# Kernel tuning notes

Hardware: AMD Instinct MI355X
Metric: run time of the kernel (lower is better)

Reference implementation:

```python
import jax, jax.numpy as jnp
import numpy as np

THRESH = 0.5
LENS = 0.5
DECAY = 0.2
K = 3


def _edge_norm(src, dst, n):
    # symmetric GCN normalization D^{-1/2} A D^{-1/2} (in-degree on dst)
    deg = jnp.zeros((n,), jnp.float32).at[dst].add(1.0)
    dinv = jnp.where(deg > 0, deg ** -0.5, 0.0)
    return dinv[src] * dinv[dst]


def _tag_conv(x, src, dst, norm, w, b):
    feats = [x]
    h = x
    for _ in range(K):
        msgs = h[:, src, :] * norm[None, :, None]   # [B, E, C]
        h = jnp.zeros_like(h).at[:, dst, :].add(msgs)
        feats.append(h)
    return jnp.concatenate(feats, axis=-1) @ w + b


def _act(m):
    # ActFun forward: heaviside at thresh
    return (m > THRESH).astype(m.dtype)


def _forward(data, sp_ei, tm_ei, conv1_w, conv1_b, conv2_w, conv2_b,
             fc1_w, fc1_b, tfc1_w, tfc1_b, act):
    B = data.shape[0]
    T = data.shape[-1]
    NS = data.shape[1] // 2  # 39 taxels
    # cat((data[:, :39], data[:, 39:]), dim=-2) -> [B, 39, 4, T]
    merged = jnp.concatenate([data[:, :NS], data[:, NS:]], axis=2)
    src_s, dst_s = sp_ei[0], sp_ei[1]
    norm_s = _edge_norm(src_s, dst_s, NS)
    src_t, dst_t = tm_ei[0], tm_ei[1]
    norm_t = _edge_norm(src_t, dst_t, T)
    COUT = conv1_w.shape[1]
    NC = fc1_w.shape[1]

    def spatial_step(carry, x_t):
        c_mem, c_spk, h_mem, h_spk, h_sum = carry
        c_mem = c_mem * DECAY * (1.0 - c_spk) + _tag_conv(x_t, src_s, dst_s, norm_s, conv1_w, conv1_b)
        c_spk = act(c_mem)
        h_mem = h_mem * DECAY * (1.0 - h_spk) + c_spk.reshape(B, -1) @ fc1_w + fc1_b
        h_spk = act(h_mem)
        return (c_mem, c_spk, h_mem, h_spk, h_sum + h_spk), None

    init_s = (jnp.zeros((B, NS, COUT)), jnp.zeros((B, NS, COUT)),
              jnp.zeros((B, NC)), jnp.zeros((B, NC)), jnp.zeros((B, NC)))
    xs_s = jnp.moveaxis(merged, 3, 0)  # [T, B, 39, 4]
    (_, _, _, _, h_sum), _ = jax.lax.scan(spatial_step, init_s, xs_s)
    out_spatial = h_sum / T

    def temporal_step(carry, x_s):
        t_mem, t_spk, th_mem, th_spk, th_sum = carry
        t_mem = t_mem * DECAY * (1.0 - t_spk) + _tag_conv(x_s, src_t, dst_t, norm_t, conv2_w, conv2_b)
        t_spk = act(t_mem)
        th_mem = th_mem * DECAY * (1.0 - th_spk) + t_spk.reshape(B, -1) @ tfc1_w + tfc1_b
        th_spk = act(th_mem)
        return (t_mem, t_spk, th_mem, th_spk, th_sum + th_spk), None

    init_t = (jnp.zeros((B, T, COUT)), jnp.zeros((B, T, COUT)),
              jnp.zeros((B, NC)), jnp.zeros((B, NC)), jnp.zeros((B, NC)))
    xs_t = jnp.moveaxis(merged, 1, 0).transpose(0, 1, 3, 2)  # [39, B, 325, 4]
    (_, _, _, _, th_sum), _ = jax.lax.scan(temporal_step, init_t, xs_t)
    out_temporal = th_sum / NS

    return (out_spatial + out_temporal) / 2.0


def setup_inputs():
    key = jax.random.key(0)
    ks = jax.random.split(key, 8)
    B, T, NS, CIN, COUT, NC = 256, 325, 39, 4, 64, 20
    data = jax.random.normal(ks[0], (B, 2 * NS, 2, T), jnp.float32)
    spatial_edge_index = jax.random.randint(ks[1], (2, NS * 3), 0, NS)
    t = jnp.arange(T - 1)
    temporal_edge_index = jnp.concatenate(
        [jnp.stack([t, t + 1]), jnp.stack([t + 1, t])], axis=1)  # [2, 648] chain
    conv1_w = jax.random.normal(ks[2], ((K + 1) * CIN, COUT), jnp.float32) * 0.1
    conv1_b = jnp.zeros((COUT,), jnp.float32)
    conv2_w = jax.random.normal(ks[3], ((K + 1) * CIN, COUT), jnp.float32) * 0.1
    conv2_b = jnp.zeros((COUT,), jnp.float32)
    fc1_w = jax.random.normal(ks[4], (NS * COUT, NC), jnp.float32) * 0.02
    fc1_b = jnp.zeros((NC,), jnp.float32)
    tfc1_w = jax.random.normal(ks[5], (T * COUT, NC), jnp.float32) * 0.02
    tfc1_b = jnp.zeros((NC,), jnp.float32)
    return dict(data=data, spatial_edge_index=spatial_edge_index,
                temporal_edge_index=temporal_edge_index,
                conv1_w=conv1_w, conv1_b=conv1_b, conv2_w=conv2_w, conv2_b=conv2_b,
                fc1_w=fc1_w, fc1_b=fc1_b, tfc1_w=tfc1_w, tfc1_b=tfc1_b)


def reference(data, spatial_edge_index, temporal_edge_index, conv1_w, conv1_b,
              conv2_w, conv2_b, fc1_w, fc1_b, tfc1_w, tfc1_b):
    return _forward(data, spatial_edge_index, temporal_edge_index,
                    conv1_w, conv1_b, conv2_w, conv2_b,
                    fc1_w, fc1_b, tfc1_w, tfc1_b, _act)
```

## Files before the change

### kernel.cpp

```cpp
#include <hip/hip_runtime.h>

typedef unsigned int u32;
typedef unsigned long long u64;
typedef short bf16x8 __attribute__((ext_vector_type(8)));
typedef float f32x4 __attribute__((ext_vector_type(4)));

#define Bc 256
#define Tc 325
#define NSc 39
#define COc 64
#define NCc 20
#define ESc 117
#define ETc 648

#define WS_ROFF_S 0
#define WS_EDGE_S 64
#define WS_DINV_S 304
#define WS_ROFF_T 352
#define WS_EDGE_T 680
#define WS_DINV_T 1976
#define WS_W1T    2304
#define WS_W2T    52224

__global__ void prep_graph(const int* __restrict__ eiS, const int* __restrict__ eiT,
                           int* __restrict__ wsI, float* __restrict__ wsF) {
  const int which = blockIdx.x;
  const int* ei = which ? eiT : eiS;
  const int nE = which ? ETc : ESc;
  const int nN = which ? Tc : NSc;
  int* roff = wsI + (which ? WS_ROFF_T : WS_ROFF_S);
  int2* edge = (int2*)(wsI + (which ? WS_EDGE_T : WS_EDGE_S));
  float* dinv = wsF + (which ? WS_DINV_T : WS_DINV_S);
  const int* src = ei;
  const int* dst = ei + nE;
  for (int n = threadIdx.x; n < nN; n += blockDim.x) {
    int deg = 0, before = 0;
    for (int e = 0; e < nE; ++e) { deg += (dst[e] == n); before += (dst[e] < n); }
    roff[n] = before;
    if (n == nN - 1) roff[nN] = before + deg;
    dinv[n] = (deg > 0) ? (1.0f / sqrtf((float)deg)) : 0.0f;
  }
  __syncthreads();
  for (int n = threadIdx.x; n < nN; n += blockDim.x) {
    int cur = roff[n];
    float dn = dinv[n];
    for (int e = 0; e < nE; ++e) {
      if (dst[e] == n) {
        edge[cur] = make_int2(src[e], __float_as_int(dinv[src[e]] * dn));
        ++cur;
      }
    }
  }
}

__global__ void prep_w(const float* __restrict__ w1, float* __restrict__ w1T,
                       const float* __restrict__ w2, float* __restrict__ w2T) {
  int i = blockIdx.x * 256 + threadIdx.x;
  if (i < NCc * Tc * COc) {
    int j = i / (Tc * COc);
    int p = i - j * (Tc * COc);
    w2T[i] = w2[p * NCc + j];
  }
  if (i < NCc * NSc * COc) {
    int j = i / (NSc * COc);
    int p = i - j * (NSc * COc);
    w1T[i] = w1[p * NCc + j];
  }
}

__global__ __launch_bounds__(512) __attribute__((amdgpu_waves_per_eu(2, 2)))
void lif_fused(const float* __restrict__ data,
               const int* __restrict__ roffSg, const int2* __restrict__ edgeSg,
               const int* __restrict__ roffTg, const int2* __restrict__ edgeTg,
               const float* __restrict__ c1w, const float* __restrict__ c1b,
               const float* __restrict__ c2w, const float* __restrict__ c2b,
               const float* __restrict__ w1T, const float* __restrict__ f1b,
               const float* __restrict__ tf1w, const float* __restrict__ tf1b,
               float* __restrict__ out)
{
  __shared__ u64 spk[NSc * Tc];
  __shared__ __align__(16) float fAB[13000];
  __shared__ float partials[520];
  __shared__ float outS_l[NCc];
  __shared__ int roffS[NSc + 1];
  __shared__ int2 edgeS[ESc];
  __shared__ int roffT[Tc + 1];
  __shared__ int2 edgeT[ETc];

  const int tid = threadIdx.x;
  const int lane = tid & 63;
  const int wv = tid >> 6;
  const int b = blockIdx.x;
  const int lhalf = lane >> 5;
  const int lbit = lane & 31;
  const float* dbase = data + (size_t)b * (2 * NSc * 2 * Tc);

  for (int i = tid; i < NSc + 1; i += 512) roffS[i] = roffSg[i];
  for (int i = tid; i < ESc; i += 512) edgeS[i] = edgeSg[i];
  for (int i = tid; i < Tc + 1; i += 512) roffT[i] = roffTg[i];
  for (int i = tid; i < ETc; i += 512) edgeT[i] = edgeTg[i];

  const int jg = wv >> 1, ih = wv & 1;
  const int ja = wv, jb = wv + 8, jc = wv + 16;
  const int jag = ja / 5, jaj = ja % 5;
  const int jbg = jb / 5, jbj = jb % 5;
  const int jcg = jc / 5, jcj = jc % 5;

  {
    const float bcv = c1b[lane];
    float cm[5] = {0, 0, 0, 0, 0};
    const int iBase = ih * 20, iN = ih ? 19 : 20;
    const float* wq0 = w1T + (jg * 5 + 0) * (NSc * COc) + iBase * COc + lane;
    const float* wq1 = w1T + (jg * 5 + 1) * (NSc * COc) + iBase * COc + lane;
    const float* wq2 = w1T + (jg * 5 + 2) * (NSc * COc) + iBase * COc + lane;
    const float* wq3 = w1T + (jg * 5 + 3) * (NSc * COc) + iBase * COc + lane;
    const float* wq4 = w1T + (jg * 5 + 4) * (NSc * COc) + iBase * COc + lane;
    const float ba = f1b[ja], bb = f1b[jb];
    const float bc2 = (wv < 4) ? f1b[jc] : 0.0f;
    float hma = 0, hsa = 0, hmb = 0, hsb = 0, hmc = 0, hsc = 0;
    __syncthreads();

#pragma unroll 1
    for (int ch = 0; ch < 25; ++ch) {
      const int t0 = ch * 13;
#pragma unroll
      for (int it = 0; it < 5; ++it) {
        int idx = tid + it * 512;
        if (idx < 2496) {
          int n = idx >> 6, c = (idx >> 4) & 3, dt = idx & 15;
          float v = 0.0f;
          if (dt < 13) v = dbase[(n + (c >> 1) * NSc) * 650 + (c & 1) * 325 + t0 + dt];
          fAB[c * 624 + n * 16 + dt] = v;
        }
      }
      __syncthreads();
#pragma unroll
      for (int k = 1; k <= 3; ++k) {
#pragma unroll
        for (int it = 0; it < 5; ++it) {
          int idx = tid + it * 512;
          if (idx < 2496) {
            int n = idx >> 6, c = (idx >> 4) & 3, dt = idx & 15;
            float v = 0.0f;
            for (int e = roffS[n]; e < roffS[n + 1]; ++e) {
              int2 ed = edgeS[e];
              v = fmaf(__int_as_float(ed.y), fAB[((k - 1) * 4 + c) * 624 + ed.x * 16 + dt], v);
            }
            fAB[(k * 4 + c) * 624 + n * 16 + dt] = v;
          }
        }
        __syncthreads();
      }
      {
        float wcr[16];
#pragma unroll
        for (int r = 0; r < 16; ++r) wcr[r] = c1w[r * COc + lane];
#pragma unroll
        for (int q = 0; q < 5; ++q) {
          int i = wv + 8 * q;
          if (i < NSc) {
            float za[13];
#pragma unroll
            for (int dt = 0; dt < 13; ++dt) za[dt] = bcv;
#pragma unroll
            for (int r = 0; r < 16; ++r) {
              const float* fp = &fAB[r * 624 + i * 16];
              float w = wcr[r];
              float4 a0 = *(const float4*)fp;
              float4 a1 = *(const float4*)(fp + 4);
              float4 a2 = *(const float4*)(fp + 8);
              float a3 = fp[12];
              za[0] = fmaf(a0.x, w, za[0]);   za[1] = fmaf(a0.y, w, za[1]);
              za[2] = fmaf(a0.z, w, za[2]);   za[3] = fmaf(a0.w, w, za[3]);
              za[4] = fmaf(a1.x, w, za[4]);   za[5] = fmaf(a1.y, w, za[5]);
              za[6] = fmaf(a1.z, w, za[6]);   za[7] = fmaf(a1.w, w, za[7]);
              za[8] = fmaf(a2.x, w, za[8]);   za[9] = fmaf(a2.y, w, za[9]);
              za[10] = fmaf(a2.z, w, za[10]); za[11] = fmaf(a2.w, w, za[11]);
              za[12] = fmaf(a3, w, za[12]);
            }
#pragma unroll
            for (int dt = 0; dt < 13; ++dt) {
              float old = cm[q];
              float m = (old * 0.2f) * ((old > 0.5f) ? 0.0f : 1.0f) + za[dt];
              cm[q] = m;
              u64 wd = __ballot(m > 0.5f);
              if (lane == 0) spk[(t0 + dt) * NSc + i] = wd;
            }
          }
        }
      }
      __syncthreads();
      float ya[13][5];
#pragma unroll
      for (int ds = 0; ds < 13; ++ds)
#pragma unroll
        for (int jj = 0; jj < 5; ++jj) ya[ds][jj] = 0.0f;
      {
        float w0 = wq0[0], w1 = wq1[0], w2 = wq2[0], w3 = wq3[0], w4 = wq4[0];
#pragma unroll 1
        for (int ii = 0; ii < iN; ++ii) {
          const int i = iBase + ii;
          const int iin = (ii + 1 < iN) ? ii + 1 : ii;
          float nw0 = wq0[iin * COc];
          float nw1 = wq1[iin * COc];
          float nw2 = wq2[iin * COc];
          float nw3 = wq3[iin * COc];
          float nw4 = wq4[iin * COc];
#pragma unroll
          for (int ds = 0; ds < 13; ++ds) {
            u32 wrd = ((const u32*)spk)[((t0 + ds) * NSc + i) * 2 + lhalf];
            float g = (float)((wrd >> lbit) & 1u);
            ya[ds][0] = fmaf(g, w0, ya[ds][0]);
            ya[ds][1] = fmaf(g, w1, ya[ds][1]);
            ya[ds][2] = fmaf(g, w2, ya[ds][2]);
            ya[ds][3] = fmaf(g, w3, ya[ds][3]);
            ya[ds][4] = fmaf(g, w4, ya[ds][4]);
          }
          w0 = nw0; w1 = nw1; w2 = nw2; w3 = nw3; w4 = nw4;
        }
      }
#pragma unroll
      for (int off = 32; off >= 1; off >>= 1)
#pragma unroll
        for (int ds = 0; ds < 13; ++ds)
#pragma unroll
          for (int jj = 0; jj < 5; ++jj)
            ya[ds][jj] += __shfl_xor(ya[ds][jj], off, 64);
      if (lane == 0) {
#pragma unroll
        for (int ds = 0; ds < 13; ++ds)
#pragma unroll
          for (int jj = 0; jj < 5; ++jj)
            partials[(jg * 2 + ih) * 65 + ds * 5 + jj] = ya[ds][jj];
      }
      __syncthreads();
#pragma unroll
      for (int ds = 0; ds < 13; ++ds) {
        float y0 = partials[(jag * 2 + 0) * 65 + ds * 5 + jaj]
                 + partials[(jag * 2 + 1) * 65 + ds * 5 + jaj] + ba;
        hma = (hma * 0.2f) * ((hma > 0.5f) ? 0.0f : 1.0f) + y0;
        hsa += (hma > 0.5f) ? 1.0f : 0.0f;
        float y1 = partials[(jbg * 2 + 0) * 65 + ds * 5 + jbj]
                 + partials[(jbg * 2 + 1) * 65 + ds * 5 + jbj] + bb;
        hmb = (hmb * 0.2f) * ((hmb > 0.5f) ? 0.0f : 1.0f) + y1;
        hsb += (hmb > 0.5f) ? 1.0f : 0.0f;
        if (wv < 4) {
          float y2 = partials[(jcg * 2 + 0) * 65 + ds * 5 + jcj]
                   + partials[(jcg * 2 + 1) * 65 + ds * 5 + jcj] + bc2;
          hmc = (hmc * 0.2f) * ((hmc > 0.5f) ? 0.0f : 1.0f) + y2;
          hsc += (hmc > 0.5f) ? 1.0f : 0.0f;
        }
      }
      __syncthreads();
    }
    if (lane == 0) {
      outS_l[ja] = hsa / (float)Tc;
      outS_l[jb] = hsb / (float)Tc;
      if (wv < 4) outS_l[jc] = hsc / (float)Tc;
    }
  }
  __syncthreads();

  {
    float wc[16];
#pragma unroll
    for (int r = 0; r < 16; ++r) wc[r] = c2w[r * COc + lane];
    const float bcv = c2b[lane];
    float tm[41];
#pragma unroll
    for (int q = 0; q < 41; ++q) tm[q] = 0.0f;

#pragma unroll 1
    for (int pr = 0; pr < 20; ++pr) {
      const int sA = pr * 2;
      const int pN = (sA + 1 < NSc) ? 2 : 1;
      const int items = pN * 1300;
#pragma unroll
      for (int it = 0; it < 6; ++it) {
        int idx = tid + it * 512;
        if (idx < items) {
          int p = (idx >= 1300) ? 1 : 0;
          int q2 = idx - p * 1300;
          int c = q2 / 325, t = q2 - c * 325;
          fAB[p * 6500 + t * 20 + c] =
              dbase[((sA + p) + (c >> 1) * NSc) * 650 + (c & 1) * 325 + t];
        }
      }
      __syncthreads();
#pragma unroll
      for (int k = 1; k <= 3; ++k) {
#pragma unroll
        for (int it = 0; it < 6; ++it) {
          int idx = tid + it * 512;
          if (idx < items) {
            int p = (idx >= 1300) ? 1 : 0;
            int q2 = idx - p * 1300;
            int t = q2 >> 2, c = q2 & 3;
            float v = 0.0f;
            for (int e = roffT[t]; e < roffT[t + 1]; ++e) {
              int2 ed = edgeT[e];
              v = fmaf(__int_as_float(ed.y), fAB[p * 6500 + ed.x * 20 + (k - 1) * 4 + c], v);
            }
            fAB[p * 6500 + t * 20 + k * 4 + c] = v;
          }
        }
        __syncthreads();
      }
#pragma unroll
      for (int q = 0; q < 41; ++q) {
        int i = wv + 8 * q;
        if (i < Tc) {
          float m = tm[q];
#pragma unroll
          for (int p = 0; p < 2; ++p) {
            if (p < pN) {
              const float4* f4 = (const float4*)&fAB[p * 6500 + i * 20];
              float4 f0 = f4[0], f1 = f4[1], f2 = f4[2], f3 = f4[3];
              float acc = bcv;
              acc = fmaf(f0.x, wc[0], acc);  acc = fmaf(f0.y, wc[1], acc);
              acc = fmaf(f0.z, wc[2], acc);  acc = fmaf(f0.w, wc[3], acc);
              acc = fmaf(f1.x, wc[4], acc);  acc = fmaf(f1.y, wc[5], acc);
              acc = fmaf(f1.z, wc[6], acc);  acc = fmaf(f1.w, wc[7], acc);
              acc = fmaf(f2.x, wc[8], acc);  acc = fmaf(f2.y, wc[9], acc);
              acc = fmaf(f2.z, wc[10], acc); acc = fmaf(f2.w, wc[11], acc);
              acc = fmaf(f3.x, wc[12], acc); acc = fmaf(f3.y, wc[13], acc);
              acc = fmaf(f3.z, wc[14], acc); acc = fmaf(f3.w, wc[15], acc);
              m = (m * 0.2f) * ((m > 0.5f) ? 0.0f : 1.0f) + acc;
              u64 wd = __ballot(m > 0.5f);
              if (lane == 0) spk[(sA + p) * Tc + i] = wd;
            }
          }
          tm[q] = m;
        }
      }
      __syncthreads();
    }
  }

  {
    const u32* spk32 = (const u32*)spk;
    float* part = fAB;
    const int kqi = wv & 3;
    const int nt = wv >> 2;
    const int col = nt * 16 + (lane & 15);
    const int lgrp = lane >> 4;
    const int srow = lane & 15;
    const int kt0 = (kqi < 2) ? kqi * 163 : 326 + (kqi - 2) * 162;
    const int ktN = (kqi < 2) ? 163 : 162;

    f32x4 c0 = {0, 0, 0, 0}, c1 = {0, 0, 0, 0}, c2 = {0, 0, 0, 0};

#pragma unroll 1
    for (int kk = 0; kk < ktN; ++kk) {
      const int kt = kt0 + kk;
      const int kbase = kt * 32 + lgrp * 8;
      bf16x8 Bhi, Bmid, Blo;
#pragma unroll
      for (int j = 0; j < 8; ++j) {
        float w = (col < NCc) ? tf1w[(kbase + j) * NCc + col] : 0.0f;
        u32 bw = __float_as_uint(w);
        u32 hbits = bw & 0xFFFF0000u;
        float r1 = w - __uint_as_float(hbits);
        u32 mbits = __float_as_uint(r1) & 0xFFFF0000u;
        float r2 = r1 - __uint_as_float(mbits);
        Bhi[j] = (short)(hbits >> 16);
        Bmid[j] = (short)(mbits >> 16);
        Blo[j] = (short)(__float_as_uint(r2) >> 16);
      }
      const int widx = (kt >> 1);
      const int wsel = (kt & 1);
      const int shft = lgrp * 8;
#pragma unroll
      for (int mt = 0; mt < 3; ++mt) {
        int s = mt * 16 + srow;
        u32 byte = 0;
        if (s < NSc) byte = (spk32[(s * Tc + widx) * 2 + wsel] >> shft) & 0xFFu;
        bf16x8 Af;
#pragma unroll
        for (int j = 0; j < 8; ++j)
          Af[j] = (short)(((byte >> j) & 1u) ? 0x3F80 : 0);
        f32x4& cc = (mt == 0) ? c0 : ((mt == 1) ? c1 : c2);
        cc = __builtin_amdgcn_mfma_f32_16x16x32_bf16(Af, Bhi, cc, 0, 0, 0);
        cc = __builtin_amdgcn_mfma_f32_16x16x32_bf16(Af, Bmid, cc, 0, 0, 0);
        cc = __builtin_amdgcn_mfma_f32_16x16x32_bf16(Af, Blo, cc, 0, 0, 0);
      }
    }
#pragma unroll
    for (int j2 = 0; j2 < 4; ++j2) {
      int row = lgrp * 4 + j2;
      part[((nt * 4 + kqi) * 3 + 0) * 256 + row * 16 + srow] = c0[j2];
      part[((nt * 4 + kqi) * 3 + 1) * 256 + row * 16 + srow] = c1[j2];
      part[((nt * 4 + kqi) * 3 + 2) * 256 + row * 16 + srow] = c2[j2];
    }
    __syncthreads();

    const float ba = tf1b[ja], bb = tf1b[jb];
    const float bc2 = (wv < 4) ? tf1b[jc] : 0.0f;
    float hma = 0, hsa = 0, hmb = 0, hsb = 0, hmc = 0, hsc = 0;
#pragma unroll 1
    for (int s = 0; s < NSc; ++s) {
      int mt = s >> 4, row = s & 15;
      int rb = mt * 256 + row * 16;
      float y0 = ba, y1 = bb, y2 = bc2;
#pragma unroll
      for (int kq2 = 0; kq2 < 4; ++kq2) {
        y0 += part[(kq2 * 3) * 256 + rb + ja];
        y1 += part[(kq2 * 3) * 256 + rb + jb];
        if (wv < 4) y2 += part[((4 + kq2) * 3) * 256 + rb + (jc - 16)];
      }
      hma = (hma * 0.2f) * ((hma > 0.5f) ? 0.0f : 1.0f) + y0;
      hsa += (hma > 0.5f) ? 1.0f : 0.0f;
      hmb = (hmb * 0.2f) * ((hmb > 0.5f) ? 0.0f : 1.0f) + y1;
      hsb += (hmb > 0.5f) ? 1.0f : 0.0f;
      if (wv < 4) {
        hmc = (hmc * 0.2f) * ((hmc > 0.5f) ? 0.0f : 1.0f) + y2;
        hsc += (hmc > 0.5f) ? 1.0f : 0.0f;
      }
    }
    if (lane == 0) {
      out[b * NCc + ja] = (outS_l[ja] + hsa / (float)NSc) * 0.5f;
      out[b * NCc + jb] = (outS_l[jb] + hsb / (float)NSc) * 0.5f;
      if (wv < 4)
        out[b * NCc + jc] = (outS_l[jc] + hsc / (float)NSc) * 0.5f;
    }
  }
}

extern "C" void kernel_launch(void* const* d_in, const int* in_sizes, int n_in,
                              void* d_out, int out_size, void* d_ws, size_t ws_size,
                              hipStream_t stream) {
  const float* data = (const float*)d_in[0];
  const int*   eiS  = (const int*)d_in[1];
  const int*   eiT  = (const int*)d_in[2];
  const float* c1w  = (const float*)d_in[3];
  const float* c1b  = (const float*)d_in[4];
  const float* c2w  = (const float*)d_in[5];
  const float* c2b  = (const float*)d_in[6];
  const float* f1w  = (const float*)d_in[7];
  const float* f1b  = (const float*)d_in[8];
  const float* tf1w = (const float*)d_in[9];
  const float* tf1b = (const float*)d_in[10];
  float* out = (float*)d_out;
  int* wsI = (int*)d_ws;
  float* wsF = (float*)d_ws;

  prep_graph<<<2, 256, 0, stream>>>(eiS, eiT, wsI, wsF);
  prep_w<<<(NCc * Tc * COc + 255) / 256, 256, 0, stream>>>(f1w, wsF + WS_W1T,
                                                           tf1w, wsF + WS_W2T);
  lif_fused<<<Bc, 512, 0, stream>>>(data,
                                    wsI + WS_ROFF_S, (const int2*)(wsI + WS_EDGE_S),
                                    wsI + WS_ROFF_T, (const int2*)(wsI + WS_EDGE_T),
                                    c1w, c1b, c2w, c2b,
                                    wsF + WS_W1T, f1b, tf1w, tf1b,
                                    out);
}
```

Measured before the change: 1.334 ms.

## Compute spatial fc1 with split-bf16 MFMA on prepacked weight fragments

```diff
diff --git a/kernel.cpp b/kernel.cpp
--- a/kernel.cpp
+++ b/kernel.cpp
@@ -19,8 +19,7 @@
 #define WS_ROFF_T 352
 #define WS_EDGE_T 680
 #define WS_DINV_T 1976
-#define WS_W1T    2304
-#define WS_W2T    52224
+#define WS_WF1    2304
 
 __global__ void prep_graph(const int* __restrict__ eiS, const int* __restrict__ eiT,
                            int* __restrict__ wsI, float* __restrict__ wsF) {
@@ -53,18 +52,34 @@
   }
 }
 
-__global__ void prep_w(const float* __restrict__ w1, float* __restrict__ w1T,
-                       const float* __restrict__ w2, float* __restrict__ w2T) {
-  int i = blockIdx.x * 256 + threadIdx.x;
-  if (i < NCc * Tc * COc) {
-    int j = i / (Tc * COc);
-    int p = i - j * (Tc * COc);
-    w2T[i] = w2[p * NCc + j];
-  }
-  if (i < NCc * NSc * COc) {
-    int j = i / (NSc * COc);
-    int p = i - j * (NSc * COc);
-    w1T[i] = w1[p * NCc + j];
+__global__ void prep_frag(const float* __restrict__ w1, u32* __restrict__ wf1) {
+  int idx = blockIdx.x * 256 + threadIdx.x;
+  if (idx < 9984) {
+    int lane = idx & 63;
+    int tile = idx >> 6;
+    int nt = tile & 1, kt = tile >> 1;
+    int lgrp = lane >> 4, col = nt * 16 + (lane & 15);
+    u32 outw[12];
+#pragma unroll
+    for (int h = 0; h < 12; ++h) outw[h] = 0u;
+#pragma unroll
+    for (int j = 0; j < 8; ++j) {
+      int k = kt * 32 + lgrp * 8 + j;
+      float w = (col < NCc) ? w1[k * NCc + col] : 0.0f;
+      u32 bw = __float_as_uint(w);
+      u32 hbits = bw & 0xFFFF0000u;
+      float r1 = w - __uint_as_float(hbits);
+      u32 mbits = __float_as_uint(r1) & 0xFFFF0000u;
+      float r2 = r1 - __uint_as_float(mbits);
+      u32 lbits = __float_as_uint(r2) & 0xFFFF0000u;
+      int wi = j >> 1, sh = (j & 1) * 16;
+      outw[0 + wi] |= (hbits >> 16) << sh;
+      outw[4 + wi] |= (mbits >> 16) << sh;
+      outw[8 + wi] |= (lbits >> 16) << sh;
+    }
+    u32* dst = wf1 + (size_t)idx * 12;
+#pragma unroll
+    for (int h = 0; h < 12; ++h) dst[h] = outw[h];
   }
 }
 
@@ -74,13 +89,12 @@
                const int* __restrict__ roffTg, const int2* __restrict__ edgeTg,
                const float* __restrict__ c1w, const float* __restrict__ c1b,
                const float* __restrict__ c2w, const float* __restrict__ c2b,
-               const float* __restrict__ w1T, const float* __restrict__ f1b,
+               const u32* __restrict__ wf1, const float* __restrict__ f1b,
                const float* __restrict__ tf1w, const float* __restrict__ tf1b,
                float* __restrict__ out)
 {
   __shared__ u64 spk[NSc * Tc];
   __shared__ __align__(16) float fAB[13000];
-  __shared__ float partials[520];
   __shared__ float outS_l[NCc];
   __shared__ int roffS[NSc + 1];
   __shared__ int2 edgeS[ESc];
@@ -91,8 +105,6 @@
   const int lane = tid & 63;
   const int wv = tid >> 6;
   const int b = blockIdx.x;
-  const int lhalf = lane >> 5;
-  const int lbit = lane & 31;
   const float* dbase = data + (size_t)b * (2 * NSc * 2 * Tc);
 
   for (int i = tid; i < NSc + 1; i += 512) roffS[i] = roffSg[i];
@@ -100,24 +112,19 @@
   for (int i = tid; i < Tc + 1; i += 512) roffT[i] = roffTg[i];
   for (int i = tid; i < ETc; i += 512) edgeT[i] = edgeTg[i];
 
-  const int jg = wv >> 1, ih = wv & 1;
   const int ja = wv, jb = wv + 8, jc = wv + 16;
-  const int jag = ja / 5, jaj = ja % 5;
-  const int jbg = jb / 5, jbj = jb % 5;
-  const int jcg = jc / 5, jcj = jc % 5;
+  const int lgrp = lane >> 4;
+  const int srow = lane & 15;
 
   {
     const float bcv = c1b[lane];
     float cm[5] = {0, 0, 0, 0, 0};
-    const int iBase = ih * 20, iN = ih ? 19 : 20;
-    const float* wq0 = w1T + (jg * 5 + 0) * (NSc * COc) + iBase * COc + lane;
-    const float* wq1 = w1T + (jg * 5 + 1) * (NSc * COc) + iBase * COc + lane;
-    const float* wq2 = w1T + (jg * 5 + 2) * (NSc * COc) + iBase * COc + lane;
-    const float* wq3 = w1T + (jg * 5 + 3) * (NSc * COc) + iBase * COc + lane;
-    const float* wq4 = w1T + (jg * 5 + 4) * (NSc * COc) + iBase * COc + lane;
     const float ba = f1b[ja], bb = f1b[jb];
     const float bc2 = (wv < 4) ? f1b[jc] : 0.0f;
     float hma = 0, hsa = 0, hmb = 0, hsb = 0, hmc = 0, hsc = 0;
+    const int kqA = wv & 3, ntA = wv >> 2;
+    const int ktA0 = (kqA < 2) ? kqA * 20 : 40 + (kqA - 2) * 19;
+    const int ktAN = (kqA < 2) ? 20 : 19;
     __syncthreads();
 
 #pragma unroll 1
@@ -190,63 +197,49 @@
         }
       }
       __syncthreads();
-      float ya[13][5];
-#pragma unroll
-      for (int ds = 0; ds < 13; ++ds)
-#pragma unroll
-        for (int jj = 0; jj < 5; ++jj) ya[ds][jj] = 0.0f;
       {
-        float w0 = wq0[0], w1 = wq1[0], w2 = wq2[0], w3 = wq3[0], w4 = wq4[0];
+        f32x4 cA = {0, 0, 0, 0};
 #pragma unroll 1
-        for (int ii = 0; ii < iN; ++ii) {
-          const int i = iBase + ii;
-          const int iin = (ii + 1 < iN) ? ii + 1 : ii;
-          float nw0 = wq0[iin * COc];
-          float nw1 = wq1[iin * COc];
-          float nw2 = wq2[iin * COc];
-          float nw3 = wq3[iin * COc];
-          float nw4 = wq4[iin * COc];
-#pragma unroll
-          for (int ds = 0; ds < 13; ++ds) {
-            u32 wrd = ((const u32*)spk)[((t0 + ds) * NSc + i) * 2 + lhalf];
-            float g = (float)((wrd >> lbit) & 1u);
-            ya[ds][0] = fmaf(g, w0, ya[ds][0]);
-            ya[ds][1] = fmaf(g, w1, ya[ds][1]);
-            ya[ds][2] = fmaf(g, w2, ya[ds][2]);
-            ya[ds][3] = fmaf(g, w3, ya[ds][3]);
-            ya[ds][4] = fmaf(g, w4, ya[ds][4]);
-          }
-          w0 = nw0; w1 = nw1; w2 = nw2; w3 = nw3; w4 = nw4;
-        }
-      }
-#pragma unroll
-      for (int off = 32; off >= 1; off >>= 1)
-#pragma unroll
-        for (int ds = 0; ds < 13; ++ds)
-#pragma unroll
-          for (int jj = 0; jj < 5; ++jj)
-            ya[ds][jj] += __shfl_xor(ya[ds][jj], off, 64);
-      if (lane == 0) {
-#pragma unroll
-        for (int ds = 0; ds < 13; ++ds)
-#pragma unroll
-          for (int jj = 0; jj < 5; ++jj)
-            partials[(jg * 2 + ih) * 65 + ds * 5 + jj] = ya[ds][jj];
+        for (int kk = 0; kk < ktAN; ++kk) {
+          const int kt = ktA0 + kk;
+          const u32* fb = wf1 + ((size_t)(kt * 2 + ntA) * 64 + lane) * 12;
+          bf16x8 Bhi = *(const bf16x8*)(fb);
+          bf16x8 Bmid = *(const bf16x8*)(fb + 4);
+          bf16x8 Blo = *(const bf16x8*)(fb + 8);
+          const int widx = kt >> 1, wsel = kt & 1;
+          u32 byte = 0;
+          if (srow < 13)
+            byte = (((const u32*)spk)[((t0 + srow) * NSc + widx) * 2 + wsel] >> (lgrp * 8)) & 0xFFu;
+          bf16x8 Af;
+#pragma unroll
+          for (int j = 0; j < 8; ++j)
+            Af[j] = (short)(((byte >> j) & 1u) ? 0x3F80 : 0);
+          cA = __builtin_amdgcn_mfma_f32_16x16x32_bf16(Af, Bhi, cA, 0, 0, 0);
+          cA = __builtin_amdgcn_mfma_f32_16x16x32_bf16(Af, Bmid, cA, 0, 0, 0);
+          cA = __builtin_amdgcn_mfma_f32_16x16x32_bf16(Af, Blo, cA, 0, 0, 0);
+        }
+        __syncthreads();
+#pragma unroll
+        for (int r = 0; r < 4; ++r) {
+          int row = lgrp * 4 + r;
+          fAB[(ntA * 4 + kqA) * 256 + row * 16 + srow] = cA[r];
+        }
       }
       __syncthreads();
 #pragma unroll
       for (int ds = 0; ds < 13; ++ds) {
-        float y0 = partials[(jag * 2 + 0) * 65 + ds * 5 + jaj]
-                 + partials[(jag * 2 + 1) * 65 + ds * 5 + jaj] + ba;
+        float y0 = ba, y1 = bb, y2 = bc2;
+#pragma unroll
+        for (int kq2 = 0; kq2 < 4; ++kq2) {
+          y0 += fAB[kq2 * 256 + ds * 16 + ja];
+          y1 += fAB[kq2 * 256 + ds * 16 + jb];
+          if (wv < 4) y2 += fAB[(4 + kq2) * 256 + ds * 16 + (jc - 16)];
+        }
         hma = (hma * 0.2f) * ((hma > 0.5f) ? 0.0f : 1.0f) + y0;
         hsa += (hma > 0.5f) ? 1.0f : 0.0f;
-        float y1 = partials[(jbg * 2 + 0) * 65 + ds * 5 + jbj]
-                 + partials[(jbg * 2 + 1) * 65 + ds * 5 + jbj] + bb;
         hmb = (hmb * 0.2f) * ((hmb > 0.5f) ? 0.0f : 1.0f) + y1;
         hsb += (hmb > 0.5f) ? 1.0f : 0.0f;
         if (wv < 4) {
-          float y2 = partials[(jcg * 2 + 0) * 65 + ds * 5 + jcj]
-                   + partials[(jcg * 2 + 1) * 65 + ds * 5 + jcj] + bc2;
           hmc = (hmc * 0.2f) * ((hmc > 0.5f) ? 0.0f : 1.0f) + y2;
           hsc += (hmc > 0.5f) ? 1.0f : 0.0f;
         }
@@ -342,9 +335,7 @@
     float* part = fAB;
     const int kqi = wv & 3;
     const int nt = wv >> 2;
-    const int col = nt * 16 + (lane & 15);
-    const int lgrp = lane >> 4;
-    const int srow = lane & 15;
+    const int col = nt * 16 + srow;
     const int kt0 = (kqi < 2) ? kqi * 163 : 326 + (kqi - 2) * 162;
     const int ktN = (kqi < 2) ? 163 : 162;
 
@@ -442,15 +433,14 @@
   const float* tf1b = (const float*)d_in[10];
   float* out = (float*)d_out;
   int* wsI = (int*)d_ws;
-  float* wsF = (float*)d_ws;
-
-  prep_graph<<<2, 256, 0, stream>>>(eiS, eiT, wsI, wsF);
-  prep_w<<<(NCc * Tc * COc + 255) / 256, 256, 0, stream>>>(f1w, wsF + WS_W1T,
-                                                           tf1w, wsF + WS_W2T);
+  u32* wsU = (u32*)d_ws;
+
+  prep_graph<<<2, 256, 0, stream>>>(eiS, eiT, wsI, (float*)d_ws);
+  prep_frag<<<(9984 + 255) / 256, 256, 0, stream>>>(f1w, wsU + WS_WF1);
   lif_fused<<<Bc, 512, 0, stream>>>(data,
                                     wsI + WS_ROFF_S, (const int2*)(wsI + WS_EDGE_S),
                                     wsI + WS_ROFF_T, (const int2*)(wsI + WS_EDGE_T),
                                     c1w, c1b, c2w, c2b,
-                                    wsF + WS_W1T, f1b, tf1w, tf1b,
+                                    wsU + WS_WF1, f1b, tf1w, tf1b,
                                     out);
 }
```

After: 1.076 ms. 19.3% less time.
